# Kernel optimization log

Hardware: AMD Instinct MI355X
Metric: run time of the kernel (lower is better)

## Reference

```python
import jax, jax.numpy as jnp
import numpy as np

N = 50000      # nodes
E = 200000     # edges
S = 8          # edge feature dim
F_IN = 32      # node feature dim after GraphMasking
F = 32         # ECCConv channels
G = 512        # graphs in disjoint batch
P = 1024       # preference pairs
N_OUT = 1      # config['n_out']


def _ecc(x, e, src, tgt, Wk, bk, root, b):
    # edge-conditioned filters: [E, F_in, F_out]
    kern = (e @ Wk + bk).reshape(E, x.shape[1], -1)
    # gather source node feats, apply per-edge filter, scatter-sum to targets
    msgs = jnp.einsum('ei,eio->eo', x[src], kern)
    agg = jax.ops.segment_sum(msgs, tgt, num_segments=N)
    return jax.nn.relu(agg + x @ root + b)


def setup_inputs() -> dict:
    key = jax.random.key(0)
    ks = jax.random.split(key, 12)
    s = 0.1
    return {
        'x': jax.random.normal(ks[0], (N, F_IN + 1), jnp.float32),
        'e': jax.random.normal(ks[1], (E, S), jnp.float32),
        'sources': jax.random.randint(ks[2], (E,), 0, N),
        'targets': jax.random.randint(ks[3], (E,), 0, N),
        'seg': jnp.sort(jax.random.randint(ks[4], (N,), 0, G)),
        'idx_a': jax.random.randint(ks[5], (P,), 0, G),
        'idx_b': jax.random.randint(ks[6], (P,), 0, G),
        'Wk1': jax.random.normal(ks[7], (S, F_IN * F), jnp.float32) * s,
        'bk1': jnp.zeros((F_IN * F,), jnp.float32),
        'root1': jax.random.normal(ks[8], (F_IN, F), jnp.float32) * s,
        'b1': jnp.zeros((F,), jnp.float32),
        'Wk2': jax.random.normal(ks[9], (S, F * F), jnp.float32) * s,
        'bk2': jnp.zeros((F * F,), jnp.float32),
        'root2': jax.random.normal(ks[10], (F, F), jnp.float32) * s,
        'b2': jnp.zeros((F,), jnp.float32),
        'Wd': jax.random.normal(ks[11], (F, N_OUT), jnp.float32) * s,
        'bd': jnp.zeros((N_OUT,), jnp.float32),
    }


def reference(x, e, sources, targets, seg, idx_a, idx_b,
              Wk1, bk1, root1, b1, Wk2, bk2, root2, b2, Wd, bd):
    h = x[:, :-1]                         # GraphMasking: drop mask column
    h = _ecc(h, e, sources, targets, Wk1, bk1, root1, b1)
    h = _ecc(h, e, sources, targets, Wk2, bk2, root2, b2)
    # tf.cast(x, int32): truncation (exact for nonneg relu output),
    # non-differentiable like the original cast.
    h = jax.lax.stop_gradient(jnp.trunc(h))
    pooled = jax.ops.segment_sum(h, seg, num_segments=G)   # GlobalSumPool
    out = jax.nn.relu(pooled @ Wd + bd)                    # Dense(n_out, relu)
    return out[idx_b] - out[idx_a]                         # pref lookup diff
```

## Files before the change

kernel.cpp:

```cpp
#include <hip/hip_runtime.h>

#define N_NODES 50000
#define N_EDGES 200000
#define S_DIM   8
#define F_DIM   32
#define G_SEG   512
#define P_PAIRS 1024
#define A_COLS  288

__global__ __launch_bounds__(256)
void zero_pooled(float* __restrict__ pooled)
{
    const int gid = blockIdx.x * 256 + threadIdx.x;
    if (gid < G_SEG * F_DIM) pooled[gid] = 0.f;
}

template <int LAYER>
__global__ __launch_bounds__(320)
void node_gemm(const float* __restrict__ hsrc,
               const float* __restrict__ Wk, const float* __restrict__ bk,
               const float* __restrict__ root, const float* __restrict__ bias,
               float* __restrict__ A, float* __restrict__ agg)
{
    const int NB = 64;
    __shared__ float hh[NB][F_DIM];

    const int nb   = blockIdx.x * NB;
    const int nmax = (N_NODES - nb < NB) ? (N_NODES - nb) : NB;

    if (LAYER == 0) {
        for (int idx = threadIdx.x; idx < nmax * F_DIM; idx += 320) {
            const int n = idx >> 5, i = idx & 31;
            hh[n][i] = hsrc[(size_t)(nb + n) * (F_DIM + 1) + i];
        }
    } else {
        const float4* src4 = (const float4*)(hsrc + (size_t)nb * F_DIM);
        for (int idx = threadIdx.x; idx < nmax * (F_DIM / 4); idx += 320) {
            float4 v = src4[idx];
            v.x = v.x > 0.f ? v.x : 0.f;
            v.y = v.y > 0.f ? v.y : 0.f;
            v.z = v.z > 0.f ? v.z : 0.f;
            v.w = v.w > 0.f ? v.w : 0.f;
            ((float4*)hh)[idx] = v;
        }
    }
    __syncthreads();

    const int c = threadIdx.x;
    float w[F_DIM];
    float init = 0.f;
    if (c < 256) {
        const int s = c >> 5, o = c & 31;
        #pragma unroll
        for (int i = 0; i < F_DIM; ++i) w[i] = Wk[s * (F_DIM * F_DIM) + i * F_DIM + o];
    } else if (c < A_COLS) {
        const int o = c & 31;
        #pragma unroll
        for (int i = 0; i < F_DIM; ++i) w[i] = bk[i * F_DIM + o];
    } else {
        const int o = c - A_COLS;
        #pragma unroll
        for (int i = 0; i < F_DIM; ++i) w[i] = root[i * F_DIM + o];
        init = bias[o];
    }

    for (int n = 0; n < nmax; ++n) {
        const float4* hv = (const float4*)hh[n];
        float acc = init;
        #pragma unroll
        for (int i4 = 0; i4 < F_DIM / 4; ++i4) {
            float4 h4 = hv[i4];
            acc += h4.x * w[4*i4]   + h4.y * w[4*i4+1]
                 + h4.z * w[4*i4+2] + h4.w * w[4*i4+3];
        }
        if (c < A_COLS) A[(size_t)(nb + n) * A_COLS + c] = acc;
        else            agg[(size_t)(nb + n) * F_DIM + (c - A_COLS)] = acc;
    }
}

__global__ __launch_bounds__(256)
void edge_msg(const float* __restrict__ A, const float* __restrict__ evec,
              const int* __restrict__ src, const int* __restrict__ tgt,
              float* __restrict__ agg)
{
    const int gid = blockIdx.x * 256 + threadIdx.x;
    const int e   = gid >> 5;
    const int o   = gid & 31;
    if (e >= N_EDGES) return;

    const int   sn = src[e];
    const int   tn = tgt[e];
    const float* Ap = A + (size_t)sn * A_COLS + o;

    float msg = Ap[8 * F_DIM];
    #pragma unroll
    for (int s = 0; s < S_DIM; ++s)
        msg += evec[(size_t)e * S_DIM + s] * Ap[s * F_DIM];

    atomicAdd(&agg[(size_t)tn * F_DIM + o], msg);
}

__global__ __launch_bounds__(256)
void pool_kernel(const float* __restrict__ agg2, const int* __restrict__ seg,
                 float* __restrict__ pooled)
{
    const int gid = blockIdx.x * 256 + threadIdx.x;
    if (gid >= N_NODES * F_DIM) return;
    const int n = gid >> 5, o = gid & 31;
    float v = agg2[gid];
    v = v > 0.f ? v : 0.f;
    v = truncf(v);
    atomicAdd(&pooled[(size_t)seg[n] * F_DIM + o], v);
}

__global__ __launch_bounds__(512)
void head_kernel(const float* __restrict__ pooled, const float* __restrict__ Wd,
                 const float* __restrict__ bd, const int* __restrict__ ia,
                 const int* __restrict__ ib, float* __restrict__ out)
{
    __shared__ float og[G_SEG];
    const int g = threadIdx.x;
    if (g < G_SEG) {
        float acc = bd[0];
        #pragma unroll
        for (int i = 0; i < F_DIM; ++i) acc += pooled[(size_t)g * F_DIM + i] * Wd[i];
        og[g] = acc > 0.f ? acc : 0.f;
    }
    __syncthreads();
    for (int p = threadIdx.x; p < P_PAIRS; p += 512)
        out[p] = og[ib[p]] - og[ia[p]];
}

extern "C" void kernel_launch(void* const* d_in, const int* in_sizes, int n_in,
                              void* d_out, int out_size, void* d_ws, size_t ws_size,
                              hipStream_t stream)
{
    const float* x    = (const float*)d_in[0];
    const float* e    = (const float*)d_in[1];
    const int*   src  = (const int*)d_in[2];
    const int*   tgt  = (const int*)d_in[3];
    const int*   seg  = (const int*)d_in[4];
    const int*   ia   = (const int*)d_in[5];
    const int*   ib   = (const int*)d_in[6];
    const float* Wk1  = (const float*)d_in[7];
    const float* bk1  = (const float*)d_in[8];
    const float* root1= (const float*)d_in[9];
    const float* b1   = (const float*)d_in[10];
    const float* Wk2  = (const float*)d_in[11];
    const float* bk2  = (const float*)d_in[12];
    const float* root2= (const float*)d_in[13];
    const float* b2   = (const float*)d_in[14];
    const float* Wd   = (const float*)d_in[15];
    const float* bd   = (const float*)d_in[16];
    float* out = (float*)d_out;

    float* A      = (float*)d_ws;
    float* ag1    = A   + (size_t)N_NODES * A_COLS;
    float* ag2    = ag1 + (size_t)N_NODES * F_DIM;
    float* pooled = ag2 + (size_t)N_NODES * F_DIM;

    const int nblk = (N_NODES + 63) / 64;
    const int eblk = (N_EDGES * 32) / 256;

    zero_pooled<<<(G_SEG * F_DIM + 255) / 256, 256, 0, stream>>>(pooled);
    node_gemm<0><<<nblk, 320, 0, stream>>>(x,   Wk1, bk1, root1, b1, A, ag1);
    edge_msg   <<<eblk, 256, 0, stream>>>(A, e, src, tgt, ag1);
    node_gemm<1><<<nblk, 320, 0, stream>>>(ag1, Wk2, bk2, root2, b2, A, ag2);
    edge_msg   <<<eblk, 256, 0, stream>>>(A, e, src, tgt, ag2);
    pool_kernel<<<(N_NODES * F_DIM + 255) / 256, 256, 0, stream>>>(ag2, seg, pooled);
    head_kernel<<<1, 512, 0, stream>>>(pooled, Wd, bd, ia, ib, out);
}
```

Before: 164.7 us.

## Build CSR by target and aggregate edges per node without atomics

Each call now builds a CSR index grouped by target node: a degree histogram, a single-block scan and an atomic scatter of edge ids. The edge message kernels then run one wavefront per target node and sum its incoming edges in registers, with no per-element float atomics. Pooling also runs per row-chunk, accumulating consecutive nodes of the same segment before each atomic. The cost is four extra small kernels per call, including a serial one-block scan, plus indirect eid loads and load imbalance across nodes of different degree.

After: 323.1 us. 1.96x slower.

```diff
diff --git a/kernel.cpp b/kernel.cpp
--- a/kernel.cpp
+++ b/kernel.cpp
@@ -9,10 +9,61 @@
 #define A_COLS  288
 
 __global__ __launch_bounds__(256)
-void zero_pooled(float* __restrict__ pooled)
+void zero_init(int* __restrict__ deg, float* __restrict__ pooled)
 {
     const int gid = blockIdx.x * 256 + threadIdx.x;
+    if (gid < N_NODES) deg[gid] = 0;
     if (gid < G_SEG * F_DIM) pooled[gid] = 0.f;
+}
+
+__global__ __launch_bounds__(256)
+void deg_hist(const int* __restrict__ tgt, int* __restrict__ deg)
+{
+    const int e = blockIdx.x * 256 + threadIdx.x;
+    if (e < N_EDGES) atomicAdd(&deg[tgt[e]], 1);
+}
+
+__global__ __launch_bounds__(1024)
+void scan_deg(const int* __restrict__ deg, int* __restrict__ rowstart,
+              int* __restrict__ cursor)
+{
+    __shared__ int psum[1024];
+    const int t  = threadIdx.x;
+    const int CH = (N_NODES + 1023) / 1024;
+    const int base = t * CH;
+
+    int s = 0;
+    for (int i = 0; i < CH; ++i)
+        if (base + i < N_NODES) s += deg[base + i];
+    psum[t] = s;
+    __syncthreads();
+    for (int off = 1; off < 1024; off <<= 1) {
+        int v = (t >= off) ? psum[t - off] : 0;
+        __syncthreads();
+        psum[t] += v;
+        __syncthreads();
+    }
+    int excl = (t == 0) ? 0 : psum[t - 1];
+    for (int i = 0; i < CH; ++i) {
+        const int n = base + i;
+        if (n < N_NODES) {
+            rowstart[n] = excl;
+            cursor[n]   = excl;
+            excl += deg[n];
+        }
+    }
+    if (t == 0) rowstart[N_NODES] = N_EDGES;
+}
+
+__global__ __launch_bounds__(256)
+void csr_scatter(const int* __restrict__ tgt, int* __restrict__ cursor,
+                 int* __restrict__ eid)
+{
+    const int e = blockIdx.x * 256 + threadIdx.x;
+    if (e < N_EDGES) {
+        const int pos = atomicAdd(&cursor[tgt[e]], 1);
+        eid[pos] = e;
+    }
 }
 
 template <int LAYER>
@@ -79,38 +130,61 @@
 }
 
 __global__ __launch_bounds__(256)
-void edge_msg(const float* __restrict__ A, const float* __restrict__ evec,
-              const int* __restrict__ src, const int* __restrict__ tgt,
-              float* __restrict__ agg)
-{
-    const int gid = blockIdx.x * 256 + threadIdx.x;
-    const int e   = gid >> 5;
-    const int o   = gid & 31;
-    if (e >= N_EDGES) return;
-
-    const int   sn = src[e];
-    const int   tn = tgt[e];
-    const float* Ap = A + (size_t)sn * A_COLS + o;
-
-    float msg = Ap[8 * F_DIM];
-    #pragma unroll
-    for (int s = 0; s < S_DIM; ++s)
-        msg += evec[(size_t)e * S_DIM + s] * Ap[s * F_DIM];
-
-    atomicAdd(&agg[(size_t)tn * F_DIM + o], msg);
+void edge_agg(const float* __restrict__ A, const float* __restrict__ evec,
+              const int* __restrict__ src, const int* __restrict__ eid,
+              const int* __restrict__ rowstart, float* __restrict__ agg)
+{
+    const int wave = (blockIdx.x * 256 + threadIdx.x) >> 6;
+    const int lane = threadIdx.x & 63;
+    if (wave >= N_NODES) return;
+    const int n = wave;
+    const int o = lane & 31;
+    const int k = lane >> 5;
+
+    const int r0 = rowstart[n];
+    const int r1 = rowstart[n + 1];
+
+    float acc = 0.f;
+    for (int idx = r0 + k; idx < r1; idx += 2) {
+        const int   e  = eid[idx];
+        const int   sn = src[e];
+        const float* Ap = A + (size_t)sn * A_COLS + o;
+        float m = Ap[8 * F_DIM];
+        #pragma unroll
+        for (int s = 0; s < S_DIM; ++s)
+            m += evec[(size_t)e * S_DIM + s] * Ap[s * F_DIM];
+        acc += m;
+    }
+    acc += __shfl_xor(acc, 32);
+    if (k == 0) agg[(size_t)n * F_DIM + o] += acc;
 }
 
 __global__ __launch_bounds__(256)
 void pool_kernel(const float* __restrict__ agg2, const int* __restrict__ seg,
                  float* __restrict__ pooled)
 {
-    const int gid = blockIdx.x * 256 + threadIdx.x;
-    if (gid >= N_NODES * F_DIM) return;
-    const int n = gid >> 5, o = gid & 31;
-    float v = agg2[gid];
-    v = v > 0.f ? v : 0.f;
-    v = truncf(v);
-    atomicAdd(&pooled[(size_t)seg[n] * F_DIM + o], v);
+    const int o    = threadIdx.x & 31;
+    const int r    = threadIdx.x >> 5;
+    const int base = blockIdx.x * 256 + r * 32;
+
+    int   curseg = -1;
+    float acc    = 0.f;
+    for (int i = 0; i < 32; ++i) {
+        const int n = base + i;
+        if (n >= N_NODES) break;
+        const int sg = seg[n];
+        if (sg != curseg) {
+            if (curseg >= 0 && acc != 0.f)
+                atomicAdd(&pooled[(size_t)curseg * F_DIM + o], acc);
+            curseg = sg;
+            acc = 0.f;
+        }
+        float v = agg2[(size_t)n * F_DIM + o];
+        v = v > 0.f ? v : 0.f;
+        acc += truncf(v);
+    }
+    if (curseg >= 0 && acc != 0.f)
+        atomicAdd(&pooled[(size_t)curseg * F_DIM + o], acc);
 }
 
 __global__ __launch_bounds__(512)
@@ -158,15 +232,25 @@
     float* ag1    = A   + (size_t)N_NODES * A_COLS;
     float* ag2    = ag1 + (size_t)N_NODES * F_DIM;
     float* pooled = ag2 + (size_t)N_NODES * F_DIM;
+    int*   deg      = (int*)(pooled + (size_t)G_SEG * F_DIM);
+    int*   cursor   = deg + N_NODES;
+    int*   rowstart = cursor + N_NODES;
+    int*   eid      = rowstart + (N_NODES + 1);
 
     const int nblk = (N_NODES + 63) / 64;
-    const int eblk = (N_EDGES * 32) / 256;
-
-    zero_pooled<<<(G_SEG * F_DIM + 255) / 256, 256, 0, stream>>>(pooled);
+    const int eblk = (N_EDGES + 255) / 256;
+    const int ablk = (N_NODES * 64 + 255) / 256;
+
+    zero_init  <<<(N_NODES + 255) / 256, 256, 0, stream>>>(deg, pooled);
+    deg_hist   <<<eblk, 256, 0, stream>>>(tgt, deg);
+    scan_deg   <<<1, 1024, 0, stream>>>(deg, rowstart, cursor);
+    csr_scatter<<<eblk, 256, 0, stream>>>(tgt, cursor, eid);
+
     node_gemm<0><<<nblk, 320, 0, stream>>>(x,   Wk1, bk1, root1, b1, A, ag1);
-    edge_msg   <<<eblk, 256, 0, stream>>>(A, e, src, tgt, ag1);
+    edge_agg    <<<ablk, 256, 0, stream>>>(A, e, src, eid, rowstart, ag1);
     node_gemm<1><<<nblk, 320, 0, stream>>>(ag1, Wk2, bk2, root2, b2, A, ag2);
-    edge_msg   <<<eblk, 256, 0, stream>>>(A, e, src, tgt, ag2);
-    pool_kernel<<<(N_NODES * F_DIM + 255) / 256, 256, 0, stream>>>(ag2, seg, pooled);
+    edge_agg    <<<ablk, 256, 0, stream>>>(A, e, src, eid, rowstart, ag2);
+
+    pool_kernel<<<(N_NODES + 255) / 256, 256, 0, stream>>>(ag2, seg, pooled);
     head_kernel<<<1, 512, 0, stream>>>(pooled, Wd, bd, ia, ib, out);
 }
```
